# Performance work log

Measured on AMD Instinct MI355X. Metric: run time of the kernel, lower is better.

Reference implementation:

```python
import jax, jax.numpy as jnp
import numpy as np
import math

L, N, E, H = 2048, 4, 1024, 16  # seq_len, batch, embed_dim, num_heads
HD = E // H                      # head_dim = 64


def setup_inputs() -> dict:
    key = jax.random.key(0)
    ks = jax.random.split(key, 7)
    s = 1.0 / math.sqrt(E)
    return {
        "query": jax.random.normal(ks[0], (L, N, E), jnp.float32),
        "key": jax.random.normal(ks[1], (L, N, E), jnp.float32),
        "value": jax.random.normal(ks[2], (L, N, E), jnp.float32),
        "in_proj_weight": jax.random.normal(ks[3], (3 * E, E), jnp.float32) * s,
        "in_proj_bias": jax.random.normal(ks[4], (3 * E,), jnp.float32) * 0.02,
        "out_proj_weight": jax.random.normal(ks[5], (E, E), jnp.float32) * s,
        "out_proj_bias": jax.random.normal(ks[6], (E,), jnp.float32) * 0.02,
    }


def reference(query, key, value, in_proj_weight, in_proj_bias,
              out_proj_weight, out_proj_bias):
    # --- packed in-projection (q is k is v path of _in_projection_packed) ---
    # F.linear(x, W, b) = x @ W.T + b, W packed as [Wq; Wk; Wv] along dim 0.
    wq, wk, wv = jnp.split(in_proj_weight, 3, axis=0)   # each (E, E)
    bq, bk, bv = jnp.split(in_proj_bias, 3, axis=0)     # each (E,)
    q = query @ wq.T + bq   # (L, N, E)
    k = key @ wk.T + bk
    v = value @ wv.T + bv

    # --- split heads: (L, N, E) -> (N*H, L, HD), matching torch reshape/transpose ---
    def to_heads(x):
        return x.reshape(L, N * H, HD).transpose(1, 0, 2)
    q, k, v = to_heads(q), to_heads(k), to_heads(v)

    # --- scaled dot-product attention (q scaled by 1/sqrt(head_dim)) ---
    q = q / math.sqrt(HD)
    attn = jnp.einsum('bte,bse->bts', q, k)             # (N*H, L, L)
    attn = jax.nn.softmax(attn, axis=-1)
    out = jnp.einsum('bts,bse->bte', attn, v)           # (N*H, L, HD)

    # --- merge heads back to (L, N, E) ---
    out = out.transpose(1, 0, 2).reshape(L, N, E)

    # --- out-projection ---
    out = out @ out_proj_weight.T + out_proj_bias       # (L, N, E)
    return out
```

## Files before the change

kernel.cpp:

```cpp
#include <hip/hip_runtime.h>

using f16 = _Float16;
typedef _Float16 h8 __attribute__((ext_vector_type(8)));
typedef _Float16 h4 __attribute__((ext_vector_type(4)));
typedef float f32x4 __attribute__((ext_vector_type(4)));

constexpr int L_SEQ  = 2048;
constexpr int NBATCH = 4;
constexpr int EMB    = 1024;
constexpr int NHEAD  = 16;
constexpr int HDIM   = 64;
constexpr int BH     = NBATCH * NHEAD;
constexpr int MROWS  = L_SEQ * NBATCH;

#define QSCALE (0.125f * 1.44269504088896341f)

__device__ __forceinline__ void glds16(const void* g, void* l) {
  __builtin_amdgcn_global_load_lds(
      (const __attribute__((address_space(1))) void*)g,
      (__attribute__((address_space(3))) void*)l, 16, 0, 0);
}

__device__ __forceinline__ f32x4 MFMA(h8 a, h8 b, f32x4 c) {
  return __builtin_amdgcn_mfma_f32_16x16x32_f16(a, b, c, 0, 0, 0);
}

__global__ void f32_to_f16_kernel(const float* __restrict__ src, f16* __restrict__ dst, int n4) {
  int i = blockIdx.x * blockDim.x + threadIdx.x;
  int stride = gridDim.x * blockDim.x;
  for (; i < n4; i += stride) {
    float4 v = reinterpret_cast<const float4*>(src)[i];
    h4 o = { (f16)v.x, (f16)v.y, (f16)v.z, (f16)v.w };
    reinterpret_cast<h4*>(dst)[i] = o;
  }
}

template<int MODE>
__global__ __launch_bounds__(256)
void gemm_bt(const f16* __restrict__ Abase, const f16* __restrict__ Btbase,
             const float* __restrict__ biasbase, f16* __restrict__ Hbase,
             float* __restrict__ Fout)
{
  const int z = blockIdx.z;
  const f16* A  = Abase  + (size_t)z * MROWS * EMB;
  const f16* Bt = Btbase + (size_t)z * EMB * EMB;
  const float* bias = biasbase + (size_t)z * EMB;

  const int bm = blockIdx.y * 128;
  const int bn = blockIdx.x * 128;
  const int t = threadIdx.x;
  const int w = t >> 6, lane = t & 63;
  const int wr = w >> 1, wc = w & 1;
  const int l16 = lane & 15, g = lane >> 4;

  __shared__ f16 As[128][32];
  __shared__ f16 Bs[128][32];

  f32x4 acc[4][4] = {};

  const int sr  = lane >> 2;
  const int sc8 = (lane & 3) * 8;
  const f16* gA = &A [(size_t)(bm + w*32 + sr) * EMB + sc8];
  const f16* gB = &Bt[(size_t)(bn + w*32 + sr) * EMB + sc8];
  f16* lA0 = &As[w*32][0];
  f16* lA1 = &As[w*32 + 16][0];
  f16* lB0 = &Bs[w*32][0];
  f16* lB1 = &Bs[w*32 + 16][0];

  for (int k0 = 0; k0 < EMB; k0 += 32) {
    __syncthreads();
    glds16(gA + k0, lA0);
    glds16(gA + (size_t)16*EMB + k0, lA1);
    glds16(gB + k0, lB0);
    glds16(gB + (size_t)16*EMB + k0, lB1);
    __syncthreads();

    h8 af[4], bfr[4];
#pragma unroll
    for (int m = 0; m < 4; ++m) af[m]  = *(const h8*)&As[wr*64 + m*16 + l16][g*8];
#pragma unroll
    for (int n = 0; n < 4; ++n) bfr[n] = *(const h8*)&Bs[wc*64 + n*16 + l16][g*8];
    __builtin_amdgcn_s_setprio(1);
#pragma unroll
    for (int m = 0; m < 4; ++m)
#pragma unroll
      for (int n = 0; n < 4; ++n)
        acc[m][n] = __builtin_amdgcn_mfma_f32_16x16x32_f16(af[m], bfr[n], acc[m][n], 0, 0, 0);
    __builtin_amdgcn_s_setprio(0);
  }

#pragma unroll
  for (int m = 0; m < 4; ++m) {
#pragma unroll
    for (int n = 0; n < 4; ++n) {
      const int col = bn + wc*64 + n*16 + l16;
      const float bv = bias[col];
#pragma unroll
      for (int r = 0; r < 4; ++r) {
        const int row = bm + wr*64 + m*16 + g*4 + r;
        float v = acc[m][n][r] + bv;
        if (MODE == 0) {
          if (z == 0) v *= QSCALE;
          const int l = row >> 2, nn = row & 3;
          const int h = col >> 6, hd = col & 63;
          Hbase[(((size_t)z * BH + nn * NHEAD + h) * L_SEQ + l) * HDIM + hd] = (f16)v;
        } else {
          Fout[(size_t)row * EMB + col] = v;
        }
      }
    }
  }
}

__global__ __launch_bounds__(256)
void vtrans_kernel(const f16* __restrict__ V, f16* __restrict__ Vt) {
  const int b = blockIdx.y;
  const int t = threadIdx.x;
  const int d = t & 63;
  const int l0 = (blockIdx.x * 4 + (t >> 6)) * 8;
  const f16* Vb = V  + (size_t)b * L_SEQ * HDIM;
  f16* Vtb      = Vt + (size_t)b * L_SEQ * HDIM;
  h8 v;
#pragma unroll
  for (int i = 0; i < 8; ++i) v[i] = Vb[(size_t)(l0 + i) * HDIM + d];
  *(h8*)&Vtb[(size_t)d * L_SEQ + l0] = v;
}

__device__ __forceinline__ void attn5_step(
    const f16* __restrict__ Kc, const f16* __restrict__ Vc, char* Pw,
    const h8 (&qf)[2][2],
    f32x4 (&o)[2][4], f32x4 (&osum)[2],
    int l16, int g)
{
  const int sw = (l16 & 7) << 3;

  h8 kf[4][2];
#pragma unroll
  for (int kt = 0; kt < 4; ++kt)
#pragma unroll
    for (int kk = 0; kk < 2; ++kk)
      kf[kt][kk] = *(const h8*)&Kc[(kt*16 + l16)*64 + ((kk*32 + g*8) ^ sw)];

  f32x4 st[2][4];
  __builtin_amdgcn_s_setprio(1);
#pragma unroll
  for (int kt = 0; kt < 4; ++kt)
#pragma unroll
    for (int qt = 0; qt < 2; ++qt) {
      f32x4 zz = {};
      zz = MFMA(kf[kt][0], qf[qt][0], zz);
      st[qt][kt] = MFMA(kf[kt][1], qf[qt][1], zz);
    }
  __builtin_amdgcn_s_setprio(0);

  h8 vf[4][2];
#pragma unroll
  for (int dt = 0; dt < 4; ++dt)
#pragma unroll
    for (int c = 0; c < 2; ++c)
      vf[dt][c] = *(const h8*)&Vc[(dt*16 + l16)*64 + ((c*32 + g*8) ^ sw)];

#pragma unroll
  for (int qt = 0; qt < 2; ++qt) {
    const int q = qt*16 + l16;
#pragma unroll
    for (int kt = 0; kt < 4; ++kt) {
      h4 pv = { (f16)__builtin_amdgcn_exp2f(st[qt][kt][0]),
                (f16)__builtin_amdgcn_exp2f(st[qt][kt][1]),
                (f16)__builtin_amdgcn_exp2f(st[qt][kt][2]),
                (f16)__builtin_amdgcn_exp2f(st[qt][kt][3]) };
      const int byteoff = (q*128 + (kt*16 + g*4)*2) ^ ((q & 7) << 4);
      *(h4*)(Pw + byteoff) = pv;
    }
  }

  const h8 ones = { (f16)1, (f16)1, (f16)1, (f16)1, (f16)1, (f16)1, (f16)1, (f16)1 };
#pragma unroll
  for (int qt = 0; qt < 2; ++qt) {
    const int q = qt*16 + l16;
#pragma unroll
    for (int c = 0; c < 2; ++c) {
      const int byteoff = (q*128 + c*64 + g*16) ^ ((q & 7) << 4);
      h8 pf = *(const h8*)(Pw + byteoff);
      __builtin_amdgcn_s_setprio(1);
      osum[qt] = MFMA(pf, ones, osum[qt]);
#pragma unroll
      for (int dt = 0; dt < 4; ++dt)
        o[qt][dt] = MFMA(pf, vf[dt][c], o[qt][dt]);
      __builtin_amdgcn_s_setprio(0);
    }
  }
}

__global__ __launch_bounds__(256, 3)
void attn5_kernel(const f16* __restrict__ Qh, const f16* __restrict__ Kh,
                  const f16* __restrict__ Vt, f16* __restrict__ AO)
{
  const int id = blockIdx.x;
  const int b    = (id & 7) | ((id >> 7) << 3);
  const int qblk = (id >> 3) & 15;

  const int t = threadIdx.x;
  const int w = t >> 6, lane = t & 63;
  const int l16 = lane & 15, g = lane >> 4;

  const f16* Qb = Qh + (size_t)b * L_SEQ * HDIM;
  const f16* Kb = Kh + (size_t)b * L_SEQ * HDIM;
  const f16* Vb = Vt + (size_t)b * (size_t)HDIM * L_SEQ;

  __shared__ f16 Ks[2][64*64];
  __shared__ f16 Vs[2][64*64];
  __shared__ f16 Plds[4][2048];
  char* Pw = (char*)&Plds[w][0];

  const int q0 = qblk * 128 + w * 32;

  h8 qf[2][2];
#pragma unroll
  for (int qt = 0; qt < 2; ++qt)
#pragma unroll
    for (int kk = 0; kk < 2; ++kk)
      qf[qt][kk] = *(const h8*)&Qb[(size_t)(q0 + qt*16 + l16) * HDIM + kk*32 + g*8];

  const int srow = lane >> 3;
  const int scol = 8 * ((lane & 7) ^ srow);
  const int r0   = w*16 + srow;
  const f16* gK0 = Kb + (size_t)(r0    ) * HDIM + scol;
  const f16* gK1 = Kb + (size_t)(r0 + 8) * HDIM + scol;
  const f16* gV0 = Vb + (size_t)(r0    ) * L_SEQ + scol;
  const f16* gV1 = Vb + (size_t)(r0 + 8) * L_SEQ + scol;
  const int ldsw = w * 1024;

  f32x4 o[2][4] = {};
  f32x4 osum[2] = {};

  glds16(gK0, &Ks[0][ldsw]);
  glds16(gK1, &Ks[0][ldsw + 512]);
  glds16(gV0, &Vs[0][ldsw]);
  glds16(gV1, &Vs[0][ldsw + 512]);
  __syncthreads();

#pragma unroll 1
  for (int j0 = 0; j0 < L_SEQ; j0 += 128) {
    {
      const int jn = (j0 + 64) & (L_SEQ - 1);
      glds16(gK0 + (size_t)jn * HDIM, &Ks[1][ldsw]);
      glds16(gK1 + (size_t)jn * HDIM, &Ks[1][ldsw + 512]);
      glds16(gV0 + jn, &Vs[1][ldsw]);
      glds16(gV1 + jn, &Vs[1][ldsw + 512]);
      attn5_step(&Ks[0][0], &Vs[0][0], Pw, qf, o, osum, l16, g);
      __syncthreads();
    }
    {
      const int jn = (j0 + 128) & (L_SEQ - 1);
      glds16(gK0 + (size_t)jn * HDIM, &Ks[0][ldsw]);
      glds16(gK1 + (size_t)jn * HDIM, &Ks[0][ldsw + 512]);
      glds16(gV0 + jn, &Vs[0][ldsw]);
      glds16(gV1 + jn, &Vs[0][ldsw + 512]);
      attn5_step(&Ks[1][0], &Vs[1][0], Pw, qf, o, osum, l16, g);
      __syncthreads();
    }
  }

  const int nn = b >> 4, h = b & 15;
#pragma unroll
  for (int qt = 0; qt < 2; ++qt) {
#pragma unroll
    for (int r = 0; r < 4; ++r) {
      const float iv = 1.0f / osum[qt][r];
      const int lr = q0 + qt*16 + g*4 + r;
#pragma unroll
      for (int dt = 0; dt < 4; ++dt)
        AO[((size_t)lr * NBATCH + nn) * EMB + h*HDIM + dt*16 + l16] = (f16)(o[qt][dt][r] * iv);
    }
  }
}

extern "C" void kernel_launch(void* const* d_in, const int* in_sizes, int n_in,
                              void* d_out, int out_size, void* d_ws, size_t ws_size,
                              hipStream_t stream) {
  const float* query = (const float*)d_in[0];
  const float* key   = (const float*)d_in[1];
  const float* value = (const float*)d_in[2];
  const float* in_w  = (const float*)d_in[3];
  const float* in_b  = (const float*)d_in[4];
  const float* out_w = (const float*)d_in[5];
  const float* out_b = (const float*)d_in[6];
  float* out = (float*)d_out;

  char* ws = (char*)d_ws;
  size_t offH  = 0;
  size_t offX  = offH  + (size_t)3 * BH * L_SEQ * HDIM * 2;
  size_t offW  = offX  + (size_t)3 * MROWS * EMB * 2;
  size_t offWo = offW  + (size_t)3 * EMB * EMB * 2;
  size_t offAO = offWo + (size_t)EMB * EMB * 2;
  f16* Hbase = (f16*)(ws + offH);
  f16* Xb    = (f16*)(ws + offX);
  f16* Wb    = (f16*)(ws + offW);
  f16* Wob   = (f16*)(ws + offWo);
  f16* AOb   = (f16*)(ws + offAO);
  f16* Vtb   = Xb;

  auto conv = [&](const float* s, f16* d, size_t n) {
    int n4 = (int)(n / 4);
    int blocks = (n4 + 255) / 256;
    if (blocks > 4096) blocks = 4096;
    hipLaunchKernelGGL(f32_to_f16_kernel, dim3(blocks), dim3(256), 0, stream, s, d, n4);
  };
  conv(query, Xb + 0 * (size_t)MROWS * EMB, (size_t)MROWS * EMB);
  conv(key,   Xb + 1 * (size_t)MROWS * EMB, (size_t)MROWS * EMB);
  conv(value, Xb + 2 * (size_t)MROWS * EMB, (size_t)MROWS * EMB);
  conv(in_w,  Wb,  (size_t)3 * EMB * EMB);
  conv(out_w, Wob, (size_t)EMB * EMB);

  hipLaunchKernelGGL((gemm_bt<0>), dim3(EMB/128, MROWS/128, 3), dim3(256), 0, stream,
                     Xb, Wb, in_b, Hbase, (float*)nullptr);

  f16* Vh = Hbase + (size_t)2 * BH * L_SEQ * HDIM;
  hipLaunchKernelGGL(vtrans_kernel, dim3(L_SEQ/32, BH), dim3(256), 0, stream, Vh, Vtb);

  hipLaunchKernelGGL(attn5_kernel, dim3(L_SEQ/128 * BH), dim3(256), 0, stream,
                     Hbase,
                     Hbase + (size_t)BH * L_SEQ * HDIM,
                     Vtb, AOb);

  hipLaunchKernelGGL((gemm_bt<1>), dim3(EMB/128, MROWS/128, 1), dim3(256), 0, stream,
                     AOb, Wob, out_b, (f16*)nullptr, out);
}
```

Before: 236.5 us.

## Merge conversion launches and halve attention P buffer to raise occupancy

```diff
diff --git a/kernel.cpp b/kernel.cpp
--- a/kernel.cpp
+++ b/kernel.cpp
@@ -25,13 +25,28 @@
   return __builtin_amdgcn_mfma_f32_16x16x32_f16(a, b, c, 0, 0, 0);
 }
 
-__global__ void f32_to_f16_kernel(const float* __restrict__ src, f16* __restrict__ dst, int n4) {
+__global__ __launch_bounds__(256)
+void convert_all_kernel(const float* __restrict__ q, const float* __restrict__ k,
+                        const float* __restrict__ v, const float* __restrict__ w,
+                        const float* __restrict__ wo,
+                        f16* __restrict__ xq, f16* __restrict__ xk, f16* __restrict__ xv,
+                        f16* __restrict__ wb, f16* __restrict__ wob) {
+  const int NQ  = MROWS * EMB / 4;
+  const int NW  = 3 * EMB * EMB / 4;
+  const int NWO = EMB * EMB / 4;
+  const int total = 3 * NQ + NW + NWO;
   int i = blockIdx.x * blockDim.x + threadIdx.x;
-  int stride = gridDim.x * blockDim.x;
-  for (; i < n4; i += stride) {
-    float4 v = reinterpret_cast<const float4*>(src)[i];
-    h4 o = { (f16)v.x, (f16)v.y, (f16)v.z, (f16)v.w };
-    reinterpret_cast<h4*>(dst)[i] = o;
+  const int stride = gridDim.x * blockDim.x;
+  for (; i < total; i += stride) {
+    const float* s; f16* d; int j;
+    if      (i <     NQ)      { s = q;  d = xq;  j = i;              }
+    else if (i < 2 * NQ)      { s = k;  d = xk;  j = i - NQ;         }
+    else if (i < 3 * NQ)      { s = v;  d = xv;  j = i - 2 * NQ;     }
+    else if (i < 3 * NQ + NW) { s = w;  d = wb;  j = i - 3 * NQ;     }
+    else                      { s = wo; d = wob; j = i - 3 * NQ - NW; }
+    float4 t = reinterpret_cast<const float4*>(s)[j];
+    h4 o = { (f16)t.x, (f16)t.y, (f16)t.z, (f16)t.w };
+    reinterpret_cast<h4*>(d)[j] = o;
   }
 }
 
@@ -126,7 +141,7 @@
   *(h8*)&Vtb[(size_t)d * L_SEQ + l0] = v;
 }
 
-__device__ __forceinline__ void attn5_step(
+__device__ __forceinline__ void attn6_step(
     const f16* __restrict__ Kc, const f16* __restrict__ Vc, char* Pw,
     const h8 (&qf)[2][2],
     f32x4 (&o)[2][4], f32x4 (&osum)[2],
@@ -160,27 +175,22 @@
     for (int c = 0; c < 2; ++c)
       vf[dt][c] = *(const h8*)&Vc[(dt*16 + l16)*64 + ((c*32 + g*8) ^ sw)];
 
+  const h8 ones = { (f16)1, (f16)1, (f16)1, (f16)1, (f16)1, (f16)1, (f16)1, (f16)1 };
+
 #pragma unroll
   for (int qt = 0; qt < 2; ++qt) {
-    const int q = qt*16 + l16;
 #pragma unroll
     for (int kt = 0; kt < 4; ++kt) {
       h4 pv = { (f16)__builtin_amdgcn_exp2f(st[qt][kt][0]),
                 (f16)__builtin_amdgcn_exp2f(st[qt][kt][1]),
                 (f16)__builtin_amdgcn_exp2f(st[qt][kt][2]),
                 (f16)__builtin_amdgcn_exp2f(st[qt][kt][3]) };
-      const int byteoff = (q*128 + (kt*16 + g*4)*2) ^ ((q & 7) << 4);
+      const int byteoff = (l16*128 + (kt*16 + g*4)*2) ^ ((l16 & 7) << 4);
       *(h4*)(Pw + byteoff) = pv;
     }
-  }
-
-  const h8 ones = { (f16)1, (f16)1, (f16)1, (f16)1, (f16)1, (f16)1, (f16)1, (f16)1 };
-#pragma unroll
-  for (int qt = 0; qt < 2; ++qt) {
-    const int q = qt*16 + l16;
 #pragma unroll
     for (int c = 0; c < 2; ++c) {
-      const int byteoff = (q*128 + c*64 + g*16) ^ ((q & 7) << 4);
+      const int byteoff = (l16*128 + c*64 + g*16) ^ ((l16 & 7) << 4);
       h8 pf = *(const h8*)(Pw + byteoff);
       __builtin_amdgcn_s_setprio(1);
       osum[qt] = MFMA(pf, ones, osum[qt]);
@@ -192,8 +202,8 @@
   }
 }
 
-__global__ __launch_bounds__(256, 3)
-void attn5_kernel(const f16* __restrict__ Qh, const f16* __restrict__ Kh,
+__global__ __launch_bounds__(256, 4)
+void attn6_kernel(const f16* __restrict__ Qh, const f16* __restrict__ Kh,
                   const f16* __restrict__ Vt, f16* __restrict__ AO)
 {
   const int id = blockIdx.x;
@@ -210,7 +220,7 @@
 
   __shared__ f16 Ks[2][64*64];
   __shared__ f16 Vs[2][64*64];
-  __shared__ f16 Plds[4][2048];
+  __shared__ f16 Plds[4][1024];
   char* Pw = (char*)&Plds[w][0];
 
   const int q0 = qblk * 128 + w * 32;
@@ -248,7 +258,7 @@
       glds16(gK1 + (size_t)jn * HDIM, &Ks[1][ldsw + 512]);
       glds16(gV0 + jn, &Vs[1][ldsw]);
       glds16(gV1 + jn, &Vs[1][ldsw + 512]);
-      attn5_step(&Ks[0][0], &Vs[0][0], Pw, qf, o, osum, l16, g);
+      attn6_step(&Ks[0][0], &Vs[0][0], Pw, qf, o, osum, l16, g);
       __syncthreads();
     }
     {
@@ -257,7 +267,7 @@
       glds16(gK1 + (size_t)jn * HDIM, &Ks[0][ldsw + 512]);
       glds16(gV0 + jn, &Vs[0][ldsw]);
       glds16(gV1 + jn, &Vs[0][ldsw + 512]);
-      attn5_step(&Ks[1][0], &Vs[1][0], Pw, qf, o, osum, l16, g);
+      attn6_step(&Ks[1][0], &Vs[1][0], Pw, qf, o, osum, l16, g);
       __syncthreads();
     }
   }
@@ -301,17 +311,12 @@
   f16* AOb   = (f16*)(ws + offAO);
   f16* Vtb   = Xb;
 
-  auto conv = [&](const float* s, f16* d, size_t n) {
-    int n4 = (int)(n / 4);
-    int blocks = (n4 + 255) / 256;
-    if (blocks > 4096) blocks = 4096;
-    hipLaunchKernelGGL(f32_to_f16_kernel, dim3(blocks), dim3(256), 0, stream, s, d, n4);
-  };
-  conv(query, Xb + 0 * (size_t)MROWS * EMB, (size_t)MROWS * EMB);
-  conv(key,   Xb + 1 * (size_t)MROWS * EMB, (size_t)MROWS * EMB);
-  conv(value, Xb + 2 * (size_t)MROWS * EMB, (size_t)MROWS * EMB);
-  conv(in_w,  Wb,  (size_t)3 * EMB * EMB);
-  conv(out_w, Wob, (size_t)EMB * EMB);
+  hipLaunchKernelGGL(convert_all_kernel, dim3(2048), dim3(256), 0, stream,
+                     query, key, value, in_w, out_w,
+                     Xb + 0 * (size_t)MROWS * EMB,
+                     Xb + 1 * (size_t)MROWS * EMB,
+                     Xb + 2 * (size_t)MROWS * EMB,
+                     Wb, Wob);
 
   hipLaunchKernelGGL((gemm_bt<0>), dim3(EMB/128, MROWS/128, 3), dim3(256), 0, stream,
                      Xb, Wb, in_b, Hbase, (float*)nullptr);
@@ -319,7 +324,7 @@
   f16* Vh = Hbase + (size_t)2 * BH * L_SEQ * HDIM;
   hipLaunchKernelGGL(vtrans_kernel, dim3(L_SEQ/32, BH), dim3(256), 0, stream, Vh, Vtb);
 
-  hipLaunchKernelGGL(attn5_kernel, dim3(L_SEQ/128 * BH), dim3(256), 0, stream,
+  hipLaunchKernelGGL(attn6_kernel, dim3(L_SEQ/128 * BH), dim3(256), 0, stream,
                      Hbase,
                      Hbase + (size_t)BH * L_SEQ * HDIM,
                      Vtb, AOb);
```

Result: slower. 402.0 us (+70.0%).
